# Kernel optimization log

Hardware: AMD Instinct MI355X
Metric: run time of the kernel (lower is better)

## Reference

```python
import jax, jax.numpy as jnp
import numpy as np

B, S, D_IN, D_OUT, RANK, HBS, ABS = 4, 2048, 4096, 4096, 32, 128, 16


def _hadamard(n: int) -> np.ndarray:
    H = np.array([[1.0]], dtype=np.float64)
    while H.shape[0] < n:
        H = np.block([[H, H], [H, -H]])
    return (H / np.sqrt(n)).astype(np.float32)


def setup_inputs() -> dict:
    key = jax.random.key(0)
    ks = jax.random.split(key, 6)
    x = jax.random.normal(ks[0], (B, S, D_IN), dtype=jnp.float32)
    # random +/-1 sign vector (matches torch.randint(0,2)*2-1)
    S_in = (jax.random.randint(ks[1], (D_IN,), 0, 2) * 2 - 1).astype(jnp.float32)
    H_block = jnp.asarray(_hadamard(HBS))  # orthonormal block Hadamard
    w_quantized = jax.random.normal(ks[2], (D_OUT, D_IN), dtype=jnp.float32) * 0.02
    lora_a = jax.random.normal(ks[3], (RANK, D_IN), dtype=jnp.float32) * 0.01
    lora_b = jax.random.normal(ks[4], (D_OUT, RANK), dtype=jnp.float32) * 0.01
    bias = jax.random.normal(ks[5], (D_OUT,), dtype=jnp.float32) * 0.01
    return {"x": x, "S_in": S_in, "H_block": H_block, "w_quantized": w_quantized,
            "lora_a": lora_a, "lora_b": lora_b, "bias": bias}


def _quantize_nvfp4(x, block_size=ABS):
    # per-block (size 16) NVFP4 fake-quant; numel here is divisible by block_size
    levels = jnp.array([0.0, 0.5, 1.0, 1.5, 2.0, 3.0, 4.0, 6.0], dtype=x.dtype)
    shape = x.shape
    xf = x.reshape(-1, block_size)
    amax = jnp.maximum(jnp.max(jnp.abs(xf), axis=-1, keepdims=True), 1e-12)
    scale = amax / 6.0
    x_norm = jnp.abs(xf) / scale
    idx = jnp.argmin(jnp.abs(x_norm[..., None] - levels), axis=-1)  # snap to grid
    xq = jnp.sign(xf) * levels[idx] * scale
    return xq.reshape(shape)


def _hadamard_rotate(x, S_in, H_block):
    # sign flip then block-diagonal Hadamard on the last dim
    shape = x.shape
    x_s = x * S_in
    x3 = x_s.reshape(*shape[:-1], shape[-1] // HBS, HBS)
    return (x3 @ H_block).reshape(shape)


def reference(x, S_in, H_block, w_quantized, lora_a, lora_b, bias):
    x_rot = _hadamard_rotate(x, S_in, H_block)          # [B,S,D_IN]
    x_q = _quantize_nvfp4(x_rot)                        # NVFP4 fake-quant activations
    out = jnp.einsum('bsd,od->bso', x_q, w_quantized)   # main GEMM
    # LoRA correction on the (unquantized) rotated activations
    out = out + jnp.einsum('bsr,or->bso', jnp.einsum('bsd,rd->bsr', x_rot, lora_a), lora_b)
    out = out + bias
    return out
```

## Files before the change

kernel.cpp:

```cpp
#include <hip/hip_runtime.h>

#define M_ROWS 8192
#define DIN    4096
#define DOUT   4096
#define RANK   32
#define KAUG   4128

typedef __attribute__((ext_vector_type(8))) short short8;
typedef __attribute__((ext_vector_type(4))) float floatx4;

__device__ __forceinline__ unsigned short f2bf(float f) {
    unsigned int u = __float_as_uint(f);
    unsigned int r = (u + 0x7FFFu + ((u >> 16) & 1u)) >> 16;
    return (unsigned short)r;
}

__global__ __launch_bounds__(256) void rot_quant_kernel(
    const float* __restrict__ x, const float* __restrict__ sgn,
    const float* __restrict__ lora_a, unsigned short* __restrict__ xaug)
{
    __shared__ float xs[4096];
    __shared__ float tred[RANK][9];

    const int row = blockIdx.x;
    const int t = threadIdx.x;
    const float* xr = x + (size_t)row * DIN;

    #pragma unroll
    for (int it = 0; it < 4; ++it) {
        int i4 = it * 256 + t;
        float4 v = ((const float4*)xr)[i4];
        float4 s = ((const float4*)sgn)[i4];
        v.x *= s.x; v.y *= s.y; v.z *= s.z; v.w *= s.w;
        ((float4*)xs)[i4] = v;
    }
    __syncthreads();

    for (int h = 1; h < 128; h <<= 1) {
        #pragma unroll
        for (int p = t; p < 2048; p += 256) {
            int i = ((p & ~(h - 1)) << 1) | (p & (h - 1));
            float a = xs[i], b = xs[i + h];
            xs[i] = a + b;
            xs[i + h] = a - b;
        }
        __syncthreads();
    }

    const float inv = 0.08838834764831845f;

    {
        float v[16];
        float amax = 0.f;
        #pragma unroll
        for (int j = 0; j < 16; ++j) {
            v[j] = xs[16 * t + j] * inv;
            amax = fmaxf(amax, fabsf(v[j]));
        }
        amax = fmaxf(amax, 1e-12f);
        float scale = amax / 6.0f;
        unsigned int pk[8];
        #pragma unroll
        for (int j = 0; j < 8; ++j) {
            unsigned short q2[2];
            #pragma unroll
            for (int e = 0; e < 2; ++e) {
                float vv = v[2 * j + e];
                float an = fabsf(vv) / scale;
                float lev = 0.0f;
                lev = an > 0.25f ? 0.5f : lev;
                lev = an > 0.75f ? 1.0f : lev;
                lev = an > 1.25f ? 1.5f : lev;
                lev = an > 1.75f ? 2.0f : lev;
                lev = an > 2.5f  ? 3.0f : lev;
                lev = an > 3.5f  ? 4.0f : lev;
                lev = an > 5.0f  ? 6.0f : lev;
                q2[e] = f2bf(copysignf(lev * scale, vv));
            }
            pk[j] = (unsigned int)q2[0] | ((unsigned int)q2[1] << 16);
        }
        unsigned short* orow = xaug + (size_t)row * KAUG + 16 * t;
        uint4 pk0 = make_uint4(pk[0], pk[1], pk[2], pk[3]);
        uint4 pk1 = make_uint4(pk[4], pk[5], pk[6], pk[7]);
        ((uint4*)orow)[0] = pk0;
        ((uint4*)orow)[1] = pk1;
    }

    {
        int r = t >> 3, oct = t & 7;
        const float* ar = lora_a + (size_t)r * DIN;
        float sum = 0.f;
        for (int d0 = oct * 4; d0 < DIN; d0 += 32) {
            float4 a4 = *(const float4*)(ar + d0);
            float4 x4 = *(const float4*)(xs + d0);
            sum += a4.x * x4.x + a4.y * x4.y + a4.z * x4.z + a4.w * x4.w;
        }
        tred[r][oct] = sum;
    }
    __syncthreads();
    if (t < RANK) {
        float s = 0.f;
        #pragma unroll
        for (int k = 0; k < 8; ++k) s += tred[t][k];
        s *= inv;
        xaug[(size_t)row * KAUG + DIN + t] = f2bf(s);
    }
}

__global__ __launch_bounds__(256) void cast_w_kernel(
    const float* __restrict__ w, const float* __restrict__ lora_b,
    unsigned short* __restrict__ waug)
{
    const int n = blockIdx.x;
    unsigned short* wr = waug + (size_t)n * KAUG;
    const float* wsrc = w + (size_t)n * DIN;
    #pragma unroll
    for (int j = threadIdx.x; j < DIN; j += 256) wr[j] = f2bf(wsrc[j]);
    if (threadIdx.x < RANK)
        wr[DIN + threadIdx.x] = f2bf(lora_b[(size_t)n * RANK + threadIdx.x]);
}

__global__ __launch_bounds__(256) void gemm_kernel(
    const unsigned short* __restrict__ A,
    const unsigned short* __restrict__ Bm,
    const float* __restrict__ bias,
    float* __restrict__ C)
{
    __shared__ unsigned short As[128 * 32];
    __shared__ unsigned short Bs[128 * 32];

    const int nt = blockIdx.x & 31;
    const int mt = blockIdx.x >> 5;
    const int m0 = mt * 128, n0 = nt * 128;
    const int t = threadIdx.x;
    const int wave = t >> 6, lane = t & 63;
    const int wm = wave & 1, wn = wave >> 1;
    const int lm = lane & 15, lq = lane >> 4;

    floatx4 acc[4][4] = {};

    for (int kk = 0; kk < KAUG; kk += 32) {
        __syncthreads();
        {
            const int c0 = wave * 2;
            const int r_ = (c0 << 4) + (lane >> 2);
            const int colb = (lane & 3) << 3;
            const unsigned short* ga = A + (size_t)(m0 + r_) * KAUG + kk + colb;
            __builtin_amdgcn_global_load_lds(
                (const __attribute__((address_space(1))) void*)ga,
                (__attribute__((address_space(3))) void*)(As + (c0 << 9)), 16, 0, 0);
            __builtin_amdgcn_global_load_lds(
                (const __attribute__((address_space(1))) void*)(ga + (size_t)16 * KAUG),
                (__attribute__((address_space(3))) void*)(As + ((c0 + 1) << 9)), 16, 0, 0);
            const unsigned short* gb = Bm + (size_t)(n0 + r_) * KAUG + kk + colb;
            __builtin_amdgcn_global_load_lds(
                (const __attribute__((address_space(1))) void*)gb,
                (__attribute__((address_space(3))) void*)(Bs + (c0 << 9)), 16, 0, 0);
            __builtin_amdgcn_global_load_lds(
                (const __attribute__((address_space(1))) void*)(gb + (size_t)16 * KAUG),
                (__attribute__((address_space(3))) void*)(Bs + ((c0 + 1) << 9)), 16, 0, 0);
        }
        __syncthreads();

        short8 af[4], bfr[4];
        #pragma unroll
        for (int mi = 0; mi < 4; ++mi)
            af[mi] = *(const short8*)&As[(wm * 64 + mi * 16 + lm) * 32 + lq * 8];
        #pragma unroll
        for (int ni = 0; ni < 4; ++ni)
            bfr[ni] = *(const short8*)&Bs[(wn * 64 + ni * 16 + lm) * 32 + lq * 8];
        #pragma unroll
        for (int mi = 0; mi < 4; ++mi)
            #pragma unroll
            for (int ni = 0; ni < 4; ++ni)
                acc[mi][ni] = __builtin_amdgcn_mfma_f32_16x16x32_bf16(
                    af[mi], bfr[ni], acc[mi][ni], 0, 0, 0);
    }

    float bv[4];
    #pragma unroll
    for (int ni = 0; ni < 4; ++ni)
        bv[ni] = bias[n0 + wn * 64 + ni * 16 + lm];
    #pragma unroll
    for (int mi = 0; mi < 4; ++mi) {
        #pragma unroll
        for (int ni = 0; ni < 4; ++ni) {
            const int col = n0 + wn * 64 + ni * 16 + lm;
            #pragma unroll
            for (int r = 0; r < 4; ++r) {
                const int rowm = m0 + wm * 64 + mi * 16 + lq * 4 + r;
                C[(size_t)rowm * DOUT + col] = acc[mi][ni][r] + bv[ni];
            }
        }
    }
}

extern "C" void kernel_launch(void* const* d_in, const int* in_sizes, int n_in,
                              void* d_out, int out_size, void* d_ws, size_t ws_size,
                              hipStream_t stream) {
    const float* x      = (const float*)d_in[0];
    const float* sgn    = (const float*)d_in[1];
    const float* w      = (const float*)d_in[3];
    const float* lora_a = (const float*)d_in[4];
    const float* lora_b = (const float*)d_in[5];
    const float* bias   = (const float*)d_in[6];
    float* out = (float*)d_out;

    unsigned short* xaug = (unsigned short*)d_ws;
    unsigned short* waug = xaug + (size_t)M_ROWS * KAUG;

    rot_quant_kernel<<<M_ROWS, 256, 0, stream>>>(x, sgn, lora_a, xaug);
    cast_w_kernel<<<DOUT, 256, 0, stream>>>(w, lora_b, waug);
    gemm_kernel<<<(M_ROWS / 128) * (DOUT / 128), 256, 0, stream>>>(xaug, waug, bias, out);
}
```

Measured before the change: 769.2 us.

## Register-shuffle Hadamard, multi-row LoRA-A, vectorized W cast, XCD-aware GEMM swizzle

The rotation kernel now keeps each 128-wide Hadamard transform in registers using in-thread butterflies and cross-lane shuffles, replacing shared-memory passes that each needed a barrier. It also handles four rows per block so the lora_a reads are shared across them, with the rotated rows stored in LDS as bf16. The weight cast is vectorized to float4 loads and packed 16-byte stores. The GEMM block index is remapped so consecutive blocks on the same XCD share tiles in L2. Computing the LoRA projection from bf16-rounded activations slightly changes numerics.

```diff
diff --git a/kernel.cpp b/kernel.cpp
--- a/kernel.cpp
+++ b/kernel.cpp
@@ -5,6 +5,7 @@
 #define DOUT   4096
 #define RANK   32
 #define KAUG   4128
+#define ROWS_PB 4
 
 typedef __attribute__((ext_vector_type(8))) short short8;
 typedef __attribute__((ext_vector_type(4))) float floatx4;
@@ -19,91 +20,127 @@
     const float* __restrict__ x, const float* __restrict__ sgn,
     const float* __restrict__ lora_a, unsigned short* __restrict__ xaug)
 {
-    __shared__ float xs[4096];
-    __shared__ float tred[RANK][9];
-
-    const int row = blockIdx.x;
+    __shared__ unsigned short xrot[ROWS_PB][DIN];
+    __shared__ float tred[ROWS_PB][RANK][8];
+
     const int t = threadIdx.x;
-    const float* xr = x + (size_t)row * DIN;
-
-    #pragma unroll
-    for (int it = 0; it < 4; ++it) {
-        int i4 = it * 256 + t;
-        float4 v = ((const float4*)xr)[i4];
-        float4 s = ((const float4*)sgn)[i4];
-        v.x *= s.x; v.y *= s.y; v.z *= s.z; v.w *= s.w;
-        ((float4*)xs)[i4] = v;
+    const int row0 = blockIdx.x * ROWS_PB;
+    const float inv = 0.08838834764831845f;
+
+    float sg[16];
+    #pragma unroll
+    for (int q = 0; q < 4; ++q)
+        *(float4*)&sg[4 * q] = ((const float4*)sgn)[t * 4 + q];
+
+    #pragma unroll 1
+    for (int rr = 0; rr < ROWS_PB; ++rr) {
+        const float* xr = x + (size_t)(row0 + rr) * DIN;
+        float v[16];
+        #pragma unroll
+        for (int q = 0; q < 4; ++q)
+            *(float4*)&v[4 * q] = ((const float4*)xr)[t * 4 + q];
+        #pragma unroll
+        for (int j = 0; j < 16; ++j) v[j] *= sg[j];
+
+        #pragma unroll
+        for (int h = 1; h < 16; h <<= 1) {
+            #pragma unroll
+            for (int i = 0; i < 16; ++i) {
+                if (!(i & h)) {
+                    float a = v[i], b = v[i + h];
+                    v[i] = a + b;
+                    v[i + h] = a - b;
+                }
+            }
+        }
+        #pragma unroll
+        for (int m = 1; m <= 4; m <<= 1) {
+            const bool up = (t & m) != 0;
+            #pragma unroll
+            for (int j = 0; j < 16; ++j) {
+                float o = __shfl_xor(v[j], m, 64);
+                v[j] = up ? (o - v[j]) : (v[j] + o);
+            }
+        }
+        #pragma unroll
+        for (int j = 0; j < 16; ++j) v[j] *= inv;
+
+        {
+            unsigned int xp[8];
+            #pragma unroll
+            for (int j = 0; j < 8; ++j)
+                xp[j] = (unsigned int)f2bf(v[2 * j]) |
+                        ((unsigned int)f2bf(v[2 * j + 1]) << 16);
+            *(uint4*)&xrot[rr][16 * t]     = make_uint4(xp[0], xp[1], xp[2], xp[3]);
+            *(uint4*)&xrot[rr][16 * t + 8] = make_uint4(xp[4], xp[5], xp[6], xp[7]);
+        }
+
+        {
+            float amax = 0.f;
+            #pragma unroll
+            for (int j = 0; j < 16; ++j) amax = fmaxf(amax, fabsf(v[j]));
+            amax = fmaxf(amax, 1e-12f);
+            float scale = amax / 6.0f;
+            unsigned int pk[8];
+            #pragma unroll
+            for (int j = 0; j < 8; ++j) {
+                unsigned short q2[2];
+                #pragma unroll
+                for (int e = 0; e < 2; ++e) {
+                    float vv = v[2 * j + e];
+                    float an = fabsf(vv) / scale;
+                    float lev = 0.0f;
+                    lev = an > 0.25f ? 0.5f : lev;
+                    lev = an > 0.75f ? 1.0f : lev;
+                    lev = an > 1.25f ? 1.5f : lev;
+                    lev = an > 1.75f ? 2.0f : lev;
+                    lev = an > 2.5f  ? 3.0f : lev;
+                    lev = an > 3.5f  ? 4.0f : lev;
+                    lev = an > 5.0f  ? 6.0f : lev;
+                    q2[e] = f2bf(copysignf(lev * scale, vv));
+                }
+                pk[j] = (unsigned int)q2[0] | ((unsigned int)q2[1] << 16);
+            }
+            unsigned short* orow = xaug + (size_t)(row0 + rr) * KAUG + 16 * t;
+            ((uint4*)orow)[0] = make_uint4(pk[0], pk[1], pk[2], pk[3]);
+            ((uint4*)orow)[1] = make_uint4(pk[4], pk[5], pk[6], pk[7]);
+        }
     }
     __syncthreads();
 
-    for (int h = 1; h < 128; h <<= 1) {
-        #pragma unroll
-        for (int p = t; p < 2048; p += 256) {
-            int i = ((p & ~(h - 1)) << 1) | (p & (h - 1));
-            float a = xs[i], b = xs[i + h];
-            xs[i] = a + b;
-            xs[i + h] = a - b;
-        }
-        __syncthreads();
-    }
-
-    const float inv = 0.08838834764831845f;
-
     {
-        float v[16];
-        float amax = 0.f;
-        #pragma unroll
-        for (int j = 0; j < 16; ++j) {
-            v[j] = xs[16 * t + j] * inv;
-            amax = fmaxf(amax, fabsf(v[j]));
-        }
-        amax = fmaxf(amax, 1e-12f);
-        float scale = amax / 6.0f;
-        unsigned int pk[8];
-        #pragma unroll
-        for (int j = 0; j < 8; ++j) {
-            unsigned short q2[2];
-            #pragma unroll
-            for (int e = 0; e < 2; ++e) {
-                float vv = v[2 * j + e];
-                float an = fabsf(vv) / scale;
-                float lev = 0.0f;
-                lev = an > 0.25f ? 0.5f : lev;
-                lev = an > 0.75f ? 1.0f : lev;
-                lev = an > 1.25f ? 1.5f : lev;
-                lev = an > 1.75f ? 2.0f : lev;
-                lev = an > 2.5f  ? 3.0f : lev;
-                lev = an > 3.5f  ? 4.0f : lev;
-                lev = an > 5.0f  ? 6.0f : lev;
-                q2[e] = f2bf(copysignf(lev * scale, vv));
-            }
-            pk[j] = (unsigned int)q2[0] | ((unsigned int)q2[1] << 16);
-        }
-        unsigned short* orow = xaug + (size_t)row * KAUG + 16 * t;
-        uint4 pk0 = make_uint4(pk[0], pk[1], pk[2], pk[3]);
-        uint4 pk1 = make_uint4(pk[4], pk[5], pk[6], pk[7]);
-        ((uint4*)orow)[0] = pk0;
-        ((uint4*)orow)[1] = pk1;
-    }
-
-    {
-        int r = t >> 3, oct = t & 7;
+        const int r = t >> 3, c = t & 7;
         const float* ar = lora_a + (size_t)r * DIN;
-        float sum = 0.f;
-        for (int d0 = oct * 4; d0 < DIN; d0 += 32) {
-            float4 a4 = *(const float4*)(ar + d0);
-            float4 x4 = *(const float4*)(xs + d0);
-            sum += a4.x * x4.x + a4.y * x4.y + a4.z * x4.z + a4.w * x4.w;
-        }
-        tred[r][oct] = sum;
+        float acc[ROWS_PB] = {0.f, 0.f, 0.f, 0.f};
+        const int d0 = c * 512, d1 = d0 + 512;
+        for (int d = d0; d < d1; d += 8) {
+            float4 a0 = *(const float4*)(ar + d);
+            float4 a1 = *(const float4*)(ar + d + 4);
+            #pragma unroll
+            for (int rr = 0; rr < ROWS_PB; ++rr) {
+                uint4 xb = *(const uint4*)&xrot[rr][d];
+                float x0 = __uint_as_float(xb.x << 16);
+                float x1 = __uint_as_float(xb.x & 0xFFFF0000u);
+                float x2 = __uint_as_float(xb.y << 16);
+                float x3 = __uint_as_float(xb.y & 0xFFFF0000u);
+                float x4 = __uint_as_float(xb.z << 16);
+                float x5 = __uint_as_float(xb.z & 0xFFFF0000u);
+                float x6 = __uint_as_float(xb.w << 16);
+                float x7 = __uint_as_float(xb.w & 0xFFFF0000u);
+                acc[rr] += a0.x * x0 + a0.y * x1 + a0.z * x2 + a0.w * x3 +
+                           a1.x * x4 + a1.y * x5 + a1.z * x6 + a1.w * x7;
+            }
+        }
+        #pragma unroll
+        for (int rr = 0; rr < ROWS_PB; ++rr) tred[rr][r][c] = acc[rr];
     }
     __syncthreads();
-    if (t < RANK) {
+    if (t < ROWS_PB * RANK) {
+        const int rr = t >> 5, rk = t & 31;
         float s = 0.f;
         #pragma unroll
-        for (int k = 0; k < 8; ++k) s += tred[t][k];
-        s *= inv;
-        xaug[(size_t)row * KAUG + DIN + t] = f2bf(s);
+        for (int k = 0; k < 8; ++k) s += tred[rr][rk][k];
+        xaug[(size_t)(row0 + rr) * KAUG + DIN + rk] = f2bf(s);
     }
 }
 
@@ -112,12 +149,22 @@
     unsigned short* __restrict__ waug)
 {
     const int n = blockIdx.x;
+    const int t = threadIdx.x;
     unsigned short* wr = waug + (size_t)n * KAUG;
     const float* wsrc = w + (size_t)n * DIN;
     #pragma unroll
-    for (int j = threadIdx.x; j < DIN; j += 256) wr[j] = f2bf(wsrc[j]);
-    if (threadIdx.x < RANK)
-        wr[DIN + threadIdx.x] = f2bf(lora_b[(size_t)n * RANK + threadIdx.x]);
+    for (int it = 0; it < 2; ++it) {
+        const int base = (it * 256 + t) * 8;
+        float4 a = ((const float4*)wsrc)[base >> 2];
+        float4 b = ((const float4*)wsrc)[(base >> 2) + 1];
+        unsigned int p0 = (unsigned int)f2bf(a.x) | ((unsigned int)f2bf(a.y) << 16);
+        unsigned int p1 = (unsigned int)f2bf(a.z) | ((unsigned int)f2bf(a.w) << 16);
+        unsigned int p2 = (unsigned int)f2bf(b.x) | ((unsigned int)f2bf(b.y) << 16);
+        unsigned int p3 = (unsigned int)f2bf(b.z) | ((unsigned int)f2bf(b.w) << 16);
+        *(uint4*)(wr + base) = make_uint4(p0, p1, p2, p3);
+    }
+    if (t < RANK)
+        wr[DIN + t] = f2bf(lora_b[(size_t)n * RANK + t]);
 }
 
 __global__ __launch_bounds__(256) void gemm_kernel(
@@ -129,8 +176,10 @@
     __shared__ unsigned short As[128 * 32];
     __shared__ unsigned short Bs[128 * 32];
 
-    const int nt = blockIdx.x & 31;
-    const int mt = blockIdx.x >> 5;
+    const int cpx = (int)(gridDim.x >> 3);
+    const int swz = ((int)blockIdx.x & 7) * cpx + ((int)blockIdx.x >> 3);
+    const int nt = swz & 31;
+    const int mt = swz >> 5;
     const int m0 = mt * 128, n0 = nt * 128;
     const int t = threadIdx.x;
     const int wave = t >> 6, lane = t & 63;
@@ -209,7 +258,7 @@
     unsigned short* xaug = (unsigned short*)d_ws;
     unsigned short* waug = xaug + (size_t)M_ROWS * KAUG;
 
-    rot_quant_kernel<<<M_ROWS, 256, 0, stream>>>(x, sgn, lora_a, xaug);
+    rot_quant_kernel<<<M_ROWS / ROWS_PB, 256, 0, stream>>>(x, sgn, lora_a, xaug);
     cast_w_kernel<<<DOUT, 256, 0, stream>>>(w, lora_b, waug);
     gemm_kernel<<<(M_ROWS / 128) * (DOUT / 128), 256, 0, stream>>>(xaug, waug, bias, out);
 }
```

New measurement: 821.1 us. 6.8% more time.
